# Kernel tuning notes

Measured on AMD Instinct MI355X. Metric: run time of the kernel, lower is better.

## Reference

```python
import jax, jax.numpy as jnp
import numpy as np

C = 256
CK = C // 8  # query/key projection dim

def conv1x1(x, w, b):
    # x: (B,C,H,W), w: (O,C), b: (O,)
    return jnp.einsum('bchw,oc->bohw', x, w) + b[None, :, None, None]

def conv3x3(x, w, b):
    # w: (O,C,3,3)
    y = jax.lax.conv_general_dilated(x, w, window_strides=(1, 1), padding='SAME',
                                     dimension_numbers=('NCHW', 'OIHW', 'NCHW'))
    return y + b[None, :, None, None]

def setup_inputs() -> dict:
    key = jax.random.key(0)
    ks = jax.random.split(key, 24)
    s = 0.05
    d = {
        'x1': jax.random.normal(ks[0], (4, C, 64, 64), jnp.float32),
        'x2': jax.random.normal(ks[1], (4, C, 64, 64), jnp.float32),
        'wq1': jax.random.normal(ks[2], (CK, C), jnp.float32) * s,
        'bq1': jax.random.normal(ks[3], (CK,), jnp.float32) * s,
        'wk1': jax.random.normal(ks[4], (CK, C), jnp.float32) * s,
        'bk1': jax.random.normal(ks[5], (CK,), jnp.float32) * s,
        'wv1': jax.random.normal(ks[6], (C, C), jnp.float32) * s,
        'bv1': jax.random.normal(ks[7], (C,), jnp.float32) * s,
        'wq2': jax.random.normal(ks[8], (CK, C), jnp.float32) * s,
        'bq2': jax.random.normal(ks[9], (CK,), jnp.float32) * s,
        'wk2': jax.random.normal(ks[10], (CK, C), jnp.float32) * s,
        'bk2': jax.random.normal(ks[11], (CK,), jnp.float32) * s,
        'wv2': jax.random.normal(ks[12], (C, C), jnp.float32) * s,
        'bv2': jax.random.normal(ks[13], (C,), jnp.float32) * s,
        'wd1': jax.random.normal(ks[14], (C, C), jnp.float32) * s,
        'bd1': jax.random.normal(ks[15], (C,), jnp.float32) * s,
        'wd3': jax.random.normal(ks[16], (C, C, 3, 3), jnp.float32) * s,
        'bd3': jax.random.normal(ks[17], (C,), jnp.float32) * s,
        'gamma1': jax.random.normal(ks[18], (1,), jnp.float32) * 0.5,
        'gamma2': jax.random.normal(ks[19], (1,), jnp.float32) * 0.5,
    }
    return d

def reference(x1, x2, wq1, bq1, wk1, bk1, wv1, bv1, wq2, bq2, wk2, bk2, wv2, bv2,
              wd1, bd1, wd3, bd3, gamma1, gamma2):
    B, Cc, H, W = x1.shape
    N = H * W
    # projections (1x1 convs), flattened to (B, d, N)
    q1 = conv1x1(x1, wq1, bq1).reshape(B, CK, N)
    k1 = conv1x1(x1, wk1, bk1).reshape(B, CK, N)
    v1 = conv1x1(x1, wv1, bv1).reshape(B, Cc, N)
    q2 = conv1x1(x2, wq2, bq2).reshape(B, CK, N)
    k2 = conv1x1(x2, wk2, bk2).reshape(B, CK, N)
    v2 = conv1x1(x2, wv2, bv2).reshape(B, Cc, N)
    # cross attention 1: queries from x1, keys/values from x2
    energy1 = jnp.einsum('bdi,bdj->bij', q1, k2)          # (B,N,N)
    attn1 = jax.nn.softmax(energy1, axis=-1)
    out1 = jnp.einsum('bcj,bij->bci', v2, attn1).reshape(B, Cc, H, W)
    # cross attention 2: queries from x2, keys/values from x1
    energy2 = jnp.einsum('bdi,bdj->bij', q2, k1)
    attn2 = jax.nn.softmax(energy2, axis=-1)
    out2 = jnp.einsum('bcj,bij->bci', v1, attn2).reshape(B, Cc, H, W)
    # residual conv branches + gamma-scaled skip (norm1/norm2 in source are dead code)
    out1 = out1 + conv1x1(x1, wd1, bd1) + conv3x3(x1, wd3, bd3)
    out2 = out2 + conv1x1(x2, wd1, bd1) + conv3x3(x2, wd3, bd3)
    out1 = x1 + gamma1[0] * out1
    out2 = x2 + gamma2[0] * out2
    return (out1, out2)
```

## Files before the change

### kernel.cpp

```cpp
#include <hip/hip_runtime.h>
#include <hip/hip_bf16.h>

#define CC 256
#define CKD 32
#define NN 4096
#define HH 64
#define WW 64
#define BB 4

typedef __attribute__((ext_vector_type(8))) short short8;
typedef __attribute__((ext_vector_type(4))) float floatx4;

__device__ __forceinline__ unsigned f2bf(float f) {
  union { float f; unsigned u; } v; v.f = f;
  unsigned r = v.u + 0x7fffu + ((v.u >> 16) & 1u);
  return r >> 16;
}

__global__ __launch_bounds__(256) void xpack_kernel(
    const float* __restrict__ x1, const float* __restrict__ x2,
    unsigned short* __restrict__ Xp) {
  const int t = threadIdx.x;
  const int nb = blockIdx.x, cbk = blockIdx.y, img = blockIdx.z;
  const float* X = ((img >> 2) ? x2 : x1) + (size_t)(img & 3) * CC * NN;
  const int n0 = nb * 64, c0 = cbk * 64;
  __shared__ float tile[64][65];
  const int nl = t & 63, cl0 = t >> 6;
#pragma unroll
  for (int i = 0; i < 16; ++i)
    tile[cl0 + i * 4][nl] = X[(size_t)(c0 + cl0 + i * 4) * NN + n0 + nl];
  __syncthreads();
#pragma unroll
  for (int it = 0; it < 2; ++it) {
    int id = it * 256 + t;
    int nl2 = id >> 3, cc = id & 7;
    short8 v;
#pragma unroll
    for (int j = 0; j < 8; ++j) v[j] = (short)f2bf(tile[cc * 8 + j][nl2]);
    *(short8*)(Xp + (size_t)img * NN * CC + (size_t)(n0 + nl2) * CC + c0 + cc * 8) = v;
  }
}

__global__ __launch_bounds__(256) void wpack_kernel(
    const float* __restrict__ wd1, const float* __restrict__ wd3,
    const float* __restrict__ wq1, const float* __restrict__ wk1,
    const float* __restrict__ wv1,
    const float* __restrict__ wq2, const float* __restrict__ wk2,
    const float* __restrict__ wv2,
    const float* __restrict__ bq1, const float* __restrict__ bk1,
    const float* __restrict__ bv1,
    const float* __restrict__ bq2, const float* __restrict__ bk2,
    const float* __restrict__ bv2,
    unsigned short* __restrict__ Wp, unsigned short* __restrict__ Wqkv,
    float* __restrict__ Bias) {
  const int id = blockIdx.x * 256 + threadIdx.x;
#pragma unroll
  for (int tap = 0; tap < 10; ++tap) {
    float v = (tap < 9) ? wd3[(size_t)id * 9 + tap] : wd1[id];
    Wp[(size_t)tap * (CC * CC) + id] = (unsigned short)f2bf(v);
  }
#pragma unroll
  for (int j = 0; j < 3; ++j) {
    int e = id + j * 65536;
    if (e < 2 * 320 * 256) {
      int inp = e / (320 * 256), rem = e % (320 * 256);
      int o = rem >> 8, c = rem & 255;
      float v;
      if (inp == 0)
        v = (o < 32) ? wq1[o * 256 + c]
            : (o < 64) ? wk1[(o - 32) * 256 + c] : wv1[(o - 64) * 256 + c];
      else
        v = (o < 32) ? wq2[o * 256 + c]
            : (o < 64) ? wk2[(o - 32) * 256 + c] : wv2[(o - 64) * 256 + c];
      Wqkv[e] = (unsigned short)f2bf(v);
    }
  }
  if (id < 640) {
    int inp = id / 320, o = id % 320;
    float v;
    if (inp == 0) v = (o < 32) ? bq1[o] : (o < 64) ? bk1[o - 32] : bv1[o - 64];
    else          v = (o < 32) ? bq2[o] : (o < 64) ? bk2[o - 32] : bv2[o - 64];
    Bias[id] = v;
  }
}

__global__ __launch_bounds__(256) void proj_mfma_kernel(
    const unsigned short* __restrict__ Xp, const unsigned short* __restrict__ Wqkv,
    const float* __restrict__ Bias,
    unsigned short* __restrict__ Qp1, unsigned short* __restrict__ Kp1,
    unsigned short* __restrict__ Vp1,
    unsigned short* __restrict__ Qp2, unsigned short* __restrict__ Kp2,
    unsigned short* __restrict__ Vp2) {
  const int t = threadIdx.x;
  const int w = t >> 6, lane = t & 63;
  const int l15 = lane & 15, g = lane >> 4;
  const int img = blockIdx.x, pb = blockIdx.y;
  const int pix0 = pb * 64;
  const int inp = img >> 2, b = img & 3;
  const unsigned short* Xi = Xp + (size_t)img * NN * CC;
  const unsigned short* Wb = Wqkv + (size_t)inp * 320 * CC;
  const float* Bi = Bias + inp * 320;
  unsigned short* Qp = (inp ? Qp2 : Qp1) + (size_t)b * NN * CKD;
  unsigned short* Kp = (inp ? Kp2 : Kp1) + (size_t)b * NN * CKD;
  unsigned short* Vp = (inp ? Vp2 : Vp1) + (size_t)b * NN * CC;

  __shared__ unsigned short tile[320][72];

  floatx4 acc[4][5];
#pragma unroll
  for (int mf = 0; mf < 4; ++mf)
#pragma unroll
    for (int nf = 0; nf < 5; ++nf) acc[mf][nf] = (floatx4){0.f, 0.f, 0.f, 0.f};
  const int o0w = w * 80;

#pragma unroll
  for (int cb = 0; cb < 8; ++cb) {
    short8 a[4], bfr[5];
#pragma unroll
    for (int mf = 0; mf < 4; ++mf)
      a[mf] = *(const short8*)(Xi + (size_t)(pix0 + mf * 16 + l15) * CC + cb * 32 + g * 8);
#pragma unroll
    for (int nf = 0; nf < 5; ++nf)
      bfr[nf] = *(const short8*)(Wb + (size_t)(o0w + nf * 16 + l15) * CC + cb * 32 + g * 8);
#pragma unroll
    for (int nf = 0; nf < 5; ++nf)
#pragma unroll
      for (int mf = 0; mf < 4; ++mf)
        acc[mf][nf] = __builtin_amdgcn_mfma_f32_16x16x32_bf16(
            a[mf], bfr[nf], acc[mf][nf], 0, 0, 0);
  }

#pragma unroll
  for (int nf = 0; nf < 5; ++nf) {
    float bs = Bi[o0w + nf * 16 + l15];
#pragma unroll
    for (int mf = 0; mf < 4; ++mf) {
      uint2 pk;
      pk.x = f2bf(acc[mf][nf][0] + bs) | (f2bf(acc[mf][nf][1] + bs) << 16);
      pk.y = f2bf(acc[mf][nf][2] + bs) | (f2bf(acc[mf][nf][3] + bs) << 16);
      *(uint2*)&tile[o0w + nf * 16 + l15][mf * 16 + g * 4] = pk;
    }
  }
  __syncthreads();

  {
    const int pix = t >> 2, ch = t & 3;
    short8 vq, vk;
#pragma unroll
    for (int e = 0; e < 8; ++e) {
      vq[e] = (short)tile[ch * 8 + e][pix];
      vk[e] = (short)tile[32 + ch * 8 + e][pix];
    }
    *(short8*)(Qp + (size_t)(pix0 + pix) * CKD + ch * 8) = vq;
    *(short8*)(Kp + (size_t)(pix0 + pix) * CKD + ch * 8) = vk;
  }
#pragma unroll
  for (int it = 0; it < 8; ++it) {
    short8 vv = *(const short8*)&tile[64 + t][it * 8];
    *(short8*)(Vp + ((size_t)((pix0 >> 3) + it) * CC + t) * 8) = vv;
  }
}

__global__ __launch_bounds__(256) void conv_mfma_kernel(
    const unsigned short* __restrict__ Xp, const unsigned short* __restrict__ Wp,
    const float* __restrict__ bd1, const float* __restrict__ bd3,
    float* __restrict__ R1, float* __restrict__ R2) {
  const int t = threadIdx.x;
  const int w = t >> 6, lane = t & 63;
  const int l15 = lane & 15, g = lane >> 4;
  const int ob = blockIdx.x, img = blockIdx.y, pb = blockIdx.z;
  const int o0 = ob * 128, n0 = pb * 128, y0 = pb * 2;
  const int wm = w >> 1, wn = w & 1;

  const unsigned short* Xi = Xp + (size_t)img * NN * CC;
  float* R = ((img >> 2) ? R2 : R1) + (size_t)(img & 3) * CC * NN;

  __shared__ unsigned short xs[4][66][72];
  __shared__ unsigned short ws[128][72];

  floatx4 acc[4][4];
#pragma unroll
  for (int m = 0; m < 4; ++m)
#pragma unroll
    for (int n = 0; n < 4; ++n) acc[m][n] = (floatx4){0.f, 0.f, 0.f, 0.f};

  for (int cb = 0; cb < 4; ++cb) {
    const int c0 = cb * 64;
    __syncthreads();
#pragma unroll
    for (int it = 0; it < 9; ++it) {
      int id = it * 256 + t;
      if (id < 2112) {
        int r = id / 528, rem = id % 528;
        int col = rem >> 3, cc = rem & 7;
        int y = y0 - 1 + r, x = col - 1;
        short8 v = {0, 0, 0, 0, 0, 0, 0, 0};
        if (y >= 0 && y < HH && x >= 0 && x < WW)
          v = *(const short8*)(Xi + (size_t)(y * WW + x) * CC + c0 + cc * 8);
        *(short8*)&xs[r][col][cc * 8] = v;
      }
    }
    for (int tap = 0; tap < 10; ++tap) {
      __syncthreads();
#pragma unroll
      for (int it = 0; it < 4; ++it) {
        int id = it * 256 + t;
        int ol = id >> 3, cc = id & 7;
        *(short8*)&ws[ol][cc * 8] = *(const short8*)(
            Wp + (size_t)(tap * CC + o0 + ol) * CC + c0 + cc * 8);
      }
      __syncthreads();
      const int dy = (tap < 9) ? tap / 3 - 1 : 0;
      const int dx = (tap < 9) ? tap % 3 - 1 : 0;
      const int rrow = 1 + wn + dy;
#pragma unroll
      for (int ks = 0; ks < 2; ++ks) {
        short8 af[4], bf[4];
#pragma unroll
        for (int m = 0; m < 4; ++m)
          af[m] = *(const short8*)&ws[wm * 64 + m * 16 + l15][ks * 32 + g * 8];
#pragma unroll
        for (int n = 0; n < 4; ++n)
          bf[n] = *(const short8*)&xs[rrow][1 + n * 16 + l15 + dx][ks * 32 + g * 8];
#pragma unroll
        for (int m = 0; m < 4; ++m)
#pragma unroll
          for (int n = 0; n < 4; ++n)
            acc[m][n] = __builtin_amdgcn_mfma_f32_16x16x32_bf16(
                af[m], bf[n], acc[m][n], 0, 0, 0);
      }
    }
  }

#pragma unroll
  for (int m = 0; m < 4; ++m) {
    int ob2 = o0 + wm * 64 + m * 16 + g * 4;
    float bs[4];
#pragma unroll
    for (int r = 0; r < 4; ++r) bs[r] = bd1[ob2 + r] + bd3[ob2 + r];
#pragma unroll
    for (int n = 0; n < 4; ++n) {
      int pix = n0 + wn * 64 + n * 16 + l15;
#pragma unroll
      for (int r = 0; r < 4; ++r)
        R[(size_t)(ob2 + r) * NN + pix] = acc[m][n][r] + bs[r];
    }
  }
}

__global__ __launch_bounds__(256, 2) void attn_kernel(
    const unsigned short* __restrict__ Qp1, const unsigned short* __restrict__ Kp1,
    const unsigned short* __restrict__ Qp2, const unsigned short* __restrict__ Kp2,
    const unsigned short* __restrict__ Vp1, const unsigned short* __restrict__ Vp2,
    const float* __restrict__ R1, const float* __restrict__ R2,
    const float* __restrict__ x1, const float* __restrict__ x2,
    const float* __restrict__ g1, const float* __restrict__ g2,
    float* __restrict__ out) {
  const int t = threadIdx.x;
  const int w = t >> 6, lane = t & 63;
  const int l15 = lane & 15, g = lane >> 4;
  const int att = blockIdx.x, b = blockIdx.y;
  const int i0 = blockIdx.z * 64;

  const unsigned short *Qp, *Kp, *Vp; const float *R, *x; float gamma; float* o;
  if (att == 0) { Qp = Qp1; Kp = Kp2; Vp = Vp2; R = R1; x = x1; gamma = g1[0]; o = out; }
  else          { Qp = Qp2; Kp = Kp1; Vp = Vp1; R = R2; x = x2; gamma = g2[0];
                  o = out + (size_t)BB * CC * NN; }
  Qp += (size_t)b * NN * CKD; Kp += (size_t)b * NN * CKD; Vp += (size_t)b * NN * CC;
  R += (size_t)b * CC * NN; x += (size_t)b * CC * NN; o += (size_t)b * CC * NN;

  __shared__ unsigned short p_s[2][64][72];
  __shared__ float l_s[64];

  short8 bq = *(const short8*)(Qp + (size_t)(i0 + w * 16 + l15) * CKD + g * 8);

  floatx4 acc[4][4];
#pragma unroll
  for (int a = 0; a < 4; ++a)
#pragma unroll
    for (int c = 0; c < 4; ++c) acc[a][c] = (floatx4){0.f, 0.f, 0.f, 0.f};
  float l_acc = 0.f;

  short8 kr[2][4], vr[2][8];
#pragma unroll
  for (int js = 0; js < 4; ++js)
    kr[0][js] = *(const short8*)(Kp + (size_t)(js * 16 + l15) * CKD + g * 8);
#pragma unroll
  for (int ks = 0; ks < 2; ++ks)
#pragma unroll
    for (int cs = 0; cs < 4; ++cs)
      vr[0][ks * 4 + cs] = *(const short8*)(Vp +
          ((size_t)(ks * 4 + g) * CC + (w * 64 + cs * 16 + l15)) * 8);

#pragma unroll 2
  for (int jt = 0; jt < NN / 64; ++jt) {
    const int cur = jt & 1, nxt = cur ^ 1;
    if (jt + 1 < NN / 64) {
      const size_t j0n = (size_t)(jt + 1) * 64;
#pragma unroll
      for (int js = 0; js < 4; ++js)
        kr[nxt][js] = *(const short8*)(Kp + (j0n + js * 16 + l15) * CKD + g * 8);
#pragma unroll
      for (int ks = 0; ks < 2; ++ks)
#pragma unroll
        for (int cs = 0; cs < 4; ++cs)
          vr[nxt][ks * 4 + cs] = *(const short8*)(Vp +
              (((j0n >> 3) + ks * 4 + g) * CC + (w * 64 + cs * 16 + l15)) * 8);
    }
#pragma unroll
    for (int js = 0; js < 4; ++js) {
      floatx4 z = {0.f, 0.f, 0.f, 0.f};
      floatx4 s = __builtin_amdgcn_mfma_f32_16x16x32_bf16(kr[cur][js], bq, z, 0, 0, 0);
      float p0 = __expf(s[0] - 16.f);
      float p1 = __expf(s[1] - 16.f);
      float p2 = __expf(s[2] - 16.f);
      float p3 = __expf(s[3] - 16.f);
      l_acc += (p0 + p1) + (p2 + p3);
      uint2 pk;
      pk.x = f2bf(p0) | (f2bf(p1) << 16);
      pk.y = f2bf(p2) | (f2bf(p3) << 16);
      *(uint2*)&p_s[cur][w * 16 + l15][js * 16 + g * 4] = pk;
    }
    __syncthreads();
#pragma unroll
    for (int ks = 0; ks < 2; ++ks) {
      short8 ap[4];
#pragma unroll
      for (int isub = 0; isub < 4; ++isub)
        ap[isub] = *(const short8*)&p_s[cur][isub * 16 + l15][ks * 32 + g * 8];
#pragma unroll
      for (int cs = 0; cs < 4; ++cs)
#pragma unroll
        for (int isub = 0; isub < 4; ++isub)
          acc[isub][cs] = __builtin_amdgcn_mfma_f32_16x16x32_bf16(
              ap[isub], vr[cur][ks * 4 + cs], acc[isub][cs], 0, 0, 0);
    }
  }

  l_acc += __shfl_xor(l_acc, 16);
  l_acc += __shfl_xor(l_acc, 32);
  if (g == 0) l_s[w * 16 + l15] = l_acc;
  __syncthreads();

#pragma unroll
  for (int isub = 0; isub < 4; ++isub) {
    float linv[4];
#pragma unroll
    for (int r = 0; r < 4; ++r) linv[r] = 1.f / l_s[isub * 16 + g * 4 + r];
#pragma unroll
    for (int cs = 0; cs < 4; ++cs) {
      int c = w * 64 + cs * 16 + l15;
      size_t base = (size_t)c * NN + i0 + isub * 16 + g * 4;
      float4 xr = *(const float4*)(x + base);
      float4 rr = *(const float4*)(R + base);
      float4 ov;
      ov.x = xr.x + gamma * (acc[isub][cs][0] * linv[0] + rr.x);
      ov.y = xr.y + gamma * (acc[isub][cs][1] * linv[1] + rr.y);
      ov.z = xr.z + gamma * (acc[isub][cs][2] * linv[2] + rr.z);
      ov.w = xr.w + gamma * (acc[isub][cs][3] * linv[3] + rr.w);
      *(float4*)(o + base) = ov;
    }
  }
}

extern "C" void kernel_launch(void* const* d_in, const int* in_sizes, int n_in,
                              void* d_out, int out_size, void* d_ws, size_t ws_size,
                              hipStream_t stream) {
  const float* x1  = (const float*)d_in[0];
  const float* x2  = (const float*)d_in[1];
  const float* wq1 = (const float*)d_in[2];
  const float* bq1 = (const float*)d_in[3];
  const float* wk1 = (const float*)d_in[4];
  const float* bk1 = (const float*)d_in[5];
  const float* wv1 = (const float*)d_in[6];
  const float* bv1 = (const float*)d_in[7];
  const float* wq2 = (const float*)d_in[8];
  const float* bq2 = (const float*)d_in[9];
  const float* wk2 = (const float*)d_in[10];
  const float* bk2 = (const float*)d_in[11];
  const float* wv2 = (const float*)d_in[12];
  const float* bv2 = (const float*)d_in[13];
  const float* wd1 = (const float*)d_in[14];
  const float* bd1 = (const float*)d_in[15];
  const float* wd3 = (const float*)d_in[16];
  const float* bd3 = (const float*)d_in[17];
  const float* g1  = (const float*)d_in[18];
  const float* g2  = (const float*)d_in[19];
  float* out = (float*)d_out;

  const size_t QB = (size_t)BB * NN * CKD * 2;
  const size_t VB = (size_t)BB * NN * CC * 2;
  const size_t RB = (size_t)BB * NN * CC * 4;
  const size_t XB = (size_t)2 * BB * NN * CC * 2;
  const size_t WPB = (size_t)10 * CC * CC * 2;
  const size_t WQB = (size_t)2 * 320 * CC * 2;
  char* base = (char*)d_ws;
  float* R1 = (float*)(base);
  float* R2 = (float*)(base + RB);
  unsigned short* Qp1 = (unsigned short*)(base + 2 * RB);
  unsigned short* Kp1 = (unsigned short*)(base + 2 * RB + QB);
  unsigned short* Qp2 = (unsigned short*)(base + 2 * RB + 2 * QB);
  unsigned short* Kp2 = (unsigned short*)(base + 2 * RB + 3 * QB);
  unsigned short* Vp1 = (unsigned short*)(base + 2 * RB + 4 * QB);
  unsigned short* Vp2 = (unsigned short*)(base + 2 * RB + 4 * QB + VB);
  unsigned short* Xp  = (unsigned short*)(base + 2 * RB + 4 * QB + 2 * VB);
  unsigned short* Wp  = (unsigned short*)(base + 2 * RB + 4 * QB + 2 * VB + XB);
  unsigned short* Wqkv = (unsigned short*)(base + 2 * RB + 4 * QB + 2 * VB + XB + WPB);
  float* Bias = (float*)(base + 2 * RB + 4 * QB + 2 * VB + XB + WPB + WQB);

  xpack_kernel<<<dim3(NN / 64, CC / 64, 2 * BB), 256, 0, stream>>>(x1, x2, Xp);
  wpack_kernel<<<dim3(CC * CC / 256), 256, 0, stream>>>(
      wd1, wd3, wq1, wk1, wv1, wq2, wk2, wv2,
      bq1, bk1, bv1, bq2, bk2, bv2, Wp, Wqkv, Bias);

  proj_mfma_kernel<<<dim3(2 * BB, NN / 64), 256, 0, stream>>>(
      Xp, Wqkv, Bias, Qp1, Kp1, Vp1, Qp2, Kp2, Vp2);

  conv_mfma_kernel<<<dim3(2, 2 * BB, NN / 128), 256, 0, stream>>>(
      Xp, Wp, bd1, bd3, R1, R2);

  attn_kernel<<<dim3(2, BB, NN / 64), 256, 0, stream>>>(
      Qp1, Kp1, Qp2, Kp2, Vp1, Vp2, R1, R2, x1, x2, g1, g2, out);
}
```

Before: 326.1 us.

## Fold log2e into Q weights, store conv residual as bf16, drop weight LDS staging

The LOG2E factor is folded into the query weights and biases so softmax uses the hardware exp2 with the fixed shift passed as the MFMA accumulator init. Bf16 packing uses cheaper round-half-up plus a perm instruction. The conv residual buffer R becomes bf16, halving its write and read traffic. The conv kernel also reads weights straight from global or cache into registers instead of staging them in LDS, which removes two barriers per tap, and it gets an occupancy hint of 2. The risks are lower precision in the residual and softmax, and conv weight loads that may now be uncoalesced.

```diff
diff --git a/kernel.cpp b/kernel.cpp
--- a/kernel.cpp
+++ b/kernel.cpp
@@ -8,6 +8,9 @@
 #define WW 64
 #define BB 4
 
+#define LOG2E 1.44269504088896f
+#define EXPSHIFT 23.0831203874f
+
 typedef __attribute__((ext_vector_type(8))) short short8;
 typedef __attribute__((ext_vector_type(4))) float floatx4;
 
@@ -15,6 +18,16 @@
   union { float f; unsigned u; } v; v.f = f;
   unsigned r = v.u + 0x7fffu + ((v.u >> 16) & 1u);
   return r >> 16;
+}
+__device__ __forceinline__ unsigned short f2bf_fast(float f) {
+  return (unsigned short)((__float_as_uint(f) + 0x8000u) >> 16);
+}
+__device__ __forceinline__ float fast_exp2(float x) {
+#if __has_builtin(__builtin_amdgcn_exp2f)
+  return __builtin_amdgcn_exp2f(x);
+#else
+  return __expf(x * 0.693147181f);
+#endif
 }
 
 __global__ __launch_bounds__(256) void xpack_kernel(
@@ -67,10 +80,10 @@
       int o = rem >> 8, c = rem & 255;
       float v;
       if (inp == 0)
-        v = (o < 32) ? wq1[o * 256 + c]
+        v = (o < 32) ? wq1[o * 256 + c] * LOG2E
             : (o < 64) ? wk1[(o - 32) * 256 + c] : wv1[(o - 64) * 256 + c];
       else
-        v = (o < 32) ? wq2[o * 256 + c]
+        v = (o < 32) ? wq2[o * 256 + c] * LOG2E
             : (o < 64) ? wk2[(o - 32) * 256 + c] : wv2[(o - 64) * 256 + c];
       Wqkv[e] = (unsigned short)f2bf(v);
     }
@@ -78,8 +91,10 @@
   if (id < 640) {
     int inp = id / 320, o = id % 320;
     float v;
-    if (inp == 0) v = (o < 32) ? bq1[o] : (o < 64) ? bk1[o - 32] : bv1[o - 64];
-    else          v = (o < 32) ? bq2[o] : (o < 64) ? bk2[o - 32] : bv2[o - 64];
+    if (inp == 0) v = (o < 32) ? bq1[o] * LOG2E
+                      : (o < 64) ? bk1[o - 32] : bv1[o - 64];
+    else          v = (o < 32) ? bq2[o] * LOG2E
+                      : (o < 64) ? bk2[o - 32] : bv2[o - 64];
     Bias[id] = v;
   }
 }
@@ -161,10 +176,10 @@
   }
 }
 
-__global__ __launch_bounds__(256) void conv_mfma_kernel(
+__global__ __launch_bounds__(256, 2) void conv_mfma_kernel(
     const unsigned short* __restrict__ Xp, const unsigned short* __restrict__ Wp,
     const float* __restrict__ bd1, const float* __restrict__ bd3,
-    float* __restrict__ R1, float* __restrict__ R2) {
+    unsigned short* __restrict__ R1, unsigned short* __restrict__ R2) {
   const int t = threadIdx.x;
   const int w = t >> 6, lane = t & 63;
   const int l15 = lane & 15, g = lane >> 4;
@@ -173,10 +188,9 @@
   const int wm = w >> 1, wn = w & 1;
 
   const unsigned short* Xi = Xp + (size_t)img * NN * CC;
-  float* R = ((img >> 2) ? R2 : R1) + (size_t)(img & 3) * CC * NN;
+  unsigned short* R = ((img >> 2) ? R2 : R1) + (size_t)(img & 3) * CC * NN;
 
   __shared__ unsigned short xs[4][66][72];
-  __shared__ unsigned short ws[128][72];
 
   floatx4 acc[4][4];
 #pragma unroll
@@ -200,25 +214,20 @@
         *(short8*)&xs[r][col][cc * 8] = v;
       }
     }
+    __syncthreads();
+#pragma unroll
     for (int tap = 0; tap < 10; ++tap) {
-      __syncthreads();
-#pragma unroll
-      for (int it = 0; it < 4; ++it) {
-        int id = it * 256 + t;
-        int ol = id >> 3, cc = id & 7;
-        *(short8*)&ws[ol][cc * 8] = *(const short8*)(
-            Wp + (size_t)(tap * CC + o0 + ol) * CC + c0 + cc * 8);
-      }
-      __syncthreads();
       const int dy = (tap < 9) ? tap / 3 - 1 : 0;
       const int dx = (tap < 9) ? tap % 3 - 1 : 0;
       const int rrow = 1 + wn + dy;
+      const unsigned short* wrow =
+          Wp + (size_t)(tap * CC + o0 + wm * 64 + l15) * CC + c0 + g * 8;
 #pragma unroll
       for (int ks = 0; ks < 2; ++ks) {
         short8 af[4], bf[4];
 #pragma unroll
         for (int m = 0; m < 4; ++m)
-          af[m] = *(const short8*)&ws[wm * 64 + m * 16 + l15][ks * 32 + g * 8];
+          af[m] = *(const short8*)(wrow + (size_t)(m * 16) * CC + ks * 32);
 #pragma unroll
         for (int n = 0; n < 4; ++n)
           bf[n] = *(const short8*)&xs[rrow][1 + n * 16 + l15 + dx][ks * 32 + g * 8];
@@ -243,7 +252,7 @@
       int pix = n0 + wn * 64 + n * 16 + l15;
 #pragma unroll
       for (int r = 0; r < 4; ++r)
-        R[(size_t)(ob2 + r) * NN + pix] = acc[m][n][r] + bs[r];
+        R[(size_t)(ob2 + r) * NN + pix] = f2bf_fast(acc[m][n][r] + bs[r]);
     }
   }
 }
@@ -252,7 +261,7 @@
     const unsigned short* __restrict__ Qp1, const unsigned short* __restrict__ Kp1,
     const unsigned short* __restrict__ Qp2, const unsigned short* __restrict__ Kp2,
     const unsigned short* __restrict__ Vp1, const unsigned short* __restrict__ Vp2,
-    const float* __restrict__ R1, const float* __restrict__ R2,
+    const unsigned short* __restrict__ R1, const unsigned short* __restrict__ R2,
     const float* __restrict__ x1, const float* __restrict__ x2,
     const float* __restrict__ g1, const float* __restrict__ g2,
     float* __restrict__ out) {
@@ -262,12 +271,12 @@
   const int att = blockIdx.x, b = blockIdx.y;
   const int i0 = blockIdx.z * 64;
 
-  const unsigned short *Qp, *Kp, *Vp; const float *R, *x; float gamma; float* o;
-  if (att == 0) { Qp = Qp1; Kp = Kp2; Vp = Vp2; R = R1; x = x1; gamma = g1[0]; o = out; }
-  else          { Qp = Qp2; Kp = Kp1; Vp = Vp1; R = R2; x = x2; gamma = g2[0];
+  const unsigned short *Qp, *Kp, *Vp, *Rb; const float *x; float gamma; float* o;
+  if (att == 0) { Qp = Qp1; Kp = Kp2; Vp = Vp2; Rb = R1; x = x1; gamma = g1[0]; o = out; }
+  else          { Qp = Qp2; Kp = Kp1; Vp = Vp1; Rb = R2; x = x2; gamma = g2[0];
                   o = out + (size_t)BB * CC * NN; }
   Qp += (size_t)b * NN * CKD; Kp += (size_t)b * NN * CKD; Vp += (size_t)b * NN * CC;
-  R += (size_t)b * CC * NN; x += (size_t)b * CC * NN; o += (size_t)b * CC * NN;
+  Rb += (size_t)b * CC * NN; x += (size_t)b * CC * NN; o += (size_t)b * CC * NN;
 
   __shared__ unsigned short p_s[2][64][72];
   __shared__ float l_s[64];
@@ -280,6 +289,7 @@
 #pragma unroll
     for (int c = 0; c < 4; ++c) acc[a][c] = (floatx4){0.f, 0.f, 0.f, 0.f};
   float l_acc = 0.f;
+  const floatx4 zinit = {-EXPSHIFT, -EXPSHIFT, -EXPSHIFT, -EXPSHIFT};
 
   short8 kr[2][4], vr[2][8];
 #pragma unroll
@@ -309,16 +319,19 @@
     }
 #pragma unroll
     for (int js = 0; js < 4; ++js) {
-      floatx4 z = {0.f, 0.f, 0.f, 0.f};
-      floatx4 s = __builtin_amdgcn_mfma_f32_16x16x32_bf16(kr[cur][js], bq, z, 0, 0, 0);
-      float p0 = __expf(s[0] - 16.f);
-      float p1 = __expf(s[1] - 16.f);
-      float p2 = __expf(s[2] - 16.f);
-      float p3 = __expf(s[3] - 16.f);
+      floatx4 s = __builtin_amdgcn_mfma_f32_16x16x32_bf16(kr[cur][js], bq, zinit, 0, 0, 0);
+      float p0 = fast_exp2(s[0]);
+      float p1 = fast_exp2(s[1]);
+      float p2 = fast_exp2(s[2]);
+      float p3 = fast_exp2(s[3]);
       l_acc += (p0 + p1) + (p2 + p3);
+      unsigned u0 = __float_as_uint(p0) + 0x8000u;
+      unsigned u1 = __float_as_uint(p1) + 0x8000u;
+      unsigned u2 = __float_as_uint(p2) + 0x8000u;
+      unsigned u3 = __float_as_uint(p3) + 0x8000u;
       uint2 pk;
-      pk.x = f2bf(p0) | (f2bf(p1) << 16);
-      pk.y = f2bf(p2) | (f2bf(p3) << 16);
+      pk.x = __builtin_amdgcn_perm(u1, u0, 0x07060302u);
+      pk.y = __builtin_amdgcn_perm(u3, u2, 0x07060302u);
       *(uint2*)&p_s[cur][w * 16 + l15][js * 16 + g * 4] = pk;
     }
     __syncthreads();
@@ -352,12 +365,16 @@
       int c = w * 64 + cs * 16 + l15;
       size_t base = (size_t)c * NN + i0 + isub * 16 + g * 4;
       float4 xr = *(const float4*)(x + base);
-      float4 rr = *(const float4*)(R + base);
+      uint2 rr = *(const uint2*)(Rb + base);
+      float r0 = __uint_as_float(rr.x << 16);
+      float r1 = __uint_as_float(rr.x & 0xffff0000u);
+      float r2 = __uint_as_float(rr.y << 16);
+      float r3 = __uint_as_float(rr.y & 0xffff0000u);
       float4 ov;
-      ov.x = xr.x + gamma * (acc[isub][cs][0] * linv[0] + rr.x);
-      ov.y = xr.y + gamma * (acc[isub][cs][1] * linv[1] + rr.y);
-      ov.z = xr.z + gamma * (acc[isub][cs][2] * linv[2] + rr.z);
-      ov.w = xr.w + gamma * (acc[isub][cs][3] * linv[3] + rr.w);
+      ov.x = xr.x + gamma * (acc[isub][cs][0] * linv[0] + r0);
+      ov.y = xr.y + gamma * (acc[isub][cs][1] * linv[1] + r1);
+      ov.z = xr.z + gamma * (acc[isub][cs][2] * linv[2] + r2);
+      ov.w = xr.w + gamma * (acc[isub][cs][3] * linv[3] + r3);
       *(float4*)(o + base) = ov;
     }
   }
@@ -390,13 +407,13 @@
 
   const size_t QB = (size_t)BB * NN * CKD * 2;
   const size_t VB = (size_t)BB * NN * CC * 2;
-  const size_t RB = (size_t)BB * NN * CC * 4;
+  const size_t RB = (size_t)BB * NN * CC * 2;
   const size_t XB = (size_t)2 * BB * NN * CC * 2;
   const size_t WPB = (size_t)10 * CC * CC * 2;
   const size_t WQB = (size_t)2 * 320 * CC * 2;
   char* base = (char*)d_ws;
-  float* R1 = (float*)(base);
-  float* R2 = (float*)(base + RB);
+  unsigned short* R1 = (unsigned short*)(base);
+  unsigned short* R2 = (unsigned short*)(base + RB);
   unsigned short* Qp1 = (unsigned short*)(base + 2 * RB);
   unsigned short* Kp1 = (unsigned short*)(base + 2 * RB + QB);
   unsigned short* Qp2 = (unsigned short*)(base + 2 * RB + 2 * QB);
```

Result: faster. 316.9 us (-2.8%).
